# Performance work log

Measured on AMD Instinct MI355X. Metric: run time of the kernel, lower is better.

Reference implementation:

```python
import jax, jax.numpy as jnp
import numpy as np

B, S, D, DIM = 8, 4096, 1024, 512  # batch, src nodes, dst nodes, feature dim


def setup_inputs() -> dict:
    key = jax.random.key(0)
    k1, k2, k3, k4, k5 = jax.random.split(key, 5)
    scale = 1.0 / np.sqrt(DIM)
    return {
        "src_val": jax.random.normal(k1, (B, S, DIM), dtype=jnp.float32),
        "src_state": jax.random.normal(k2, (B, S), dtype=jnp.float32),
        "dst_val": jax.random.normal(k3, (B, D, DIM), dtype=jnp.float32),
        "W_route": jax.random.normal(k4, (DIM, DIM), dtype=jnp.float32) * scale,
        "W_val": jax.random.normal(k5, (DIM, DIM), dtype=jnp.float32) * scale,
    }


def reference(src_val, src_state, dst_val, W_route, W_val):
    # Pairwise route logits: bilinear bipartite attention, [B, S, D]
    inv_sqrt_d = 1.0 / jnp.sqrt(jnp.asarray(src_val.shape[-1], src_val.dtype))
    q = jnp.einsum("bsd,de->bse", src_val, W_route)
    logits = jnp.einsum("bse,bke->bsk", q, dst_val) * inv_sqrt_d
    # route compression: softmax over dst nodes (dim=-1)
    routes = jax.nn.softmax(logits, axis=-1)
    # projections
    projected_val = jnp.einsum("bsd,de->bse", src_val, W_val)  # [B, S, DIM]
    projected_state = src_state                                 # identity state proj, [B, S]
    sender_strength = jax.nn.softplus(src_state)                # [B, S]
    # weighted routing + accumulation
    weighted_routes = routes * sender_strength[..., None]       # [B, S, D]
    delta_state = jnp.einsum("bsk,bs->bk", weighted_routes, projected_state)   # [B, D]
    delta_val = jnp.einsum("bsk,bsd->bkd", weighted_routes, projected_val)     # [B, D, DIM]
    return delta_state, delta_val
```

## Files before the change

kernel.cpp:

```cpp
#include <hip/hip_runtime.h>
#include <hip/hip_fp16.h>

#define B_   8
#define S_   4096
#define DD_  1024
#define DIM_ 512
#define SCALE 0.044194173824159216f

typedef __bf16 bf16x8 __attribute__((ext_vector_type(8)));
typedef float  floatx4 __attribute__((ext_vector_type(4)));

__device__ inline unsigned short f2bf(float f) {
    union { float f; unsigned int u; } v; v.f = f;
    unsigned int r = v.u + 0x7fffu + ((v.u >> 16) & 1u);
    return (unsigned short)(r >> 16);
}
__device__ inline float bf2f(unsigned short h) {
    union { unsigned int u; float f; } v; v.u = ((unsigned int)h) << 16;
    return v.f;
}
__device__ inline uint4 cvt8(const float* __restrict__ g) {
    float4 f0 = *(const float4*)g;
    float4 f1 = *(const float4*)(g + 4);
    unsigned short tmp[8] = {f2bf(f0.x), f2bf(f0.y), f2bf(f0.z), f2bf(f0.w),
                             f2bf(f1.x), f2bf(f1.y), f2bf(f1.z), f2bf(f1.w)};
    return *(const uint4*)tmp;
}
__device__ inline void async16(unsigned short* lds, const unsigned short* g) {
    __builtin_amdgcn_global_load_lds(
        (const __attribute__((address_space(1))) void*)g,
        (__attribute__((address_space(3))) void*)lds, 16, 0, 0);
}

template <int AF32, int BF32>
__device__ inline void mainloop(unsigned short* As, unsigned short* Bs,
                                const void* Ap, size_t lda,
                                const void* Bp, size_t ldb,
                                int kIters, floatx4 (&acc)[4][4]) {
    const int t = threadIdx.x, lane = t & 63, wave = t >> 6;
    const int rA = t >> 2, cA = (t & 3) * 8;
    const int mrow = (wave >> 1) * 64, ncol = (wave & 1) * 64;
    const int fr = lane & 15, fk = (lane >> 4) * 8;

    const unsigned short* gA16 = nullptr; const float* gA32 = nullptr;
    const unsigned short* gB16 = nullptr; const float* gB32 = nullptr;
    if (AF32) gA32 = (const float*)Ap + (size_t)rA * lda + cA;
    else      gA16 = (const unsigned short*)Ap + (size_t)rA * lda + cA;
    if (BF32) gB32 = (const float*)Bp + (size_t)rA * ldb + cA;
    else      gB16 = (const unsigned short*)Bp + (size_t)rA * ldb + cA;

    unsigned short* ldsA = As + wave * 512;
    unsigned short* ldsB = Bs + wave * 512;

    for (int kt = 0; kt < kIters; ++kt) {
        if (AF32) {
            *(uint4*)&As[t * 8]        = cvt8(gA32);
            *(uint4*)&As[2048 + t * 8] = cvt8(gA32 + 64 * lda);
            gA32 += 32;
        } else {
            async16(ldsA,        gA16);
            async16(ldsA + 2048, gA16 + 64 * lda);
            gA16 += 32;
        }
        if (BF32) {
            *(uint4*)&Bs[t * 8]        = cvt8(gB32);
            *(uint4*)&Bs[2048 + t * 8] = cvt8(gB32 + 64 * ldb);
            gB32 += 32;
        } else {
            async16(ldsB,        gB16);
            async16(ldsB + 2048, gB16 + 64 * ldb);
            gB16 += 32;
        }
        __syncthreads();
        bf16x8 af[4], bfr[4];
#pragma unroll
        for (int i = 0; i < 4; ++i)
            af[i] = *(const bf16x8*)&As[(mrow + i * 16 + fr) * 32 + fk];
#pragma unroll
        for (int j = 0; j < 4; ++j)
            bfr[j] = *(const bf16x8*)&Bs[(ncol + j * 16 + fr) * 32 + fk];
#pragma unroll
        for (int i = 0; i < 4; ++i)
#pragma unroll
            for (int j = 0; j < 4; ++j)
                acc[i][j] = __builtin_amdgcn_mfma_f32_16x16x32_bf16(af[i], bfr[j],
                                                                    acc[i][j], 0, 0, 0);
        __syncthreads();
    }
}

#define EPILOGUE_COORDS                                     \
    const int lane = threadIdx.x & 63, wave = threadIdx.x >> 6; \
    const int mrow = (wave >> 1) * 64, ncol = (wave & 1) * 64;  \
    const int col = lane & 15, q = lane >> 4;

#define ACC_INIT                                            \
    floatx4 acc[4][4];                                      \
    _Pragma("unroll") for (int i = 0; i < 4; ++i)           \
        _Pragma("unroll") for (int j = 0; j < 4; ++j)       \
            acc[i][j] = (floatx4){0.f, 0.f, 0.f, 0.f};

__global__ __launch_bounds__(256) void k_prep(const float* __restrict__ dst,
                                              unsigned short* __restrict__ dstb,
                                              const float* __restrict__ Wr,
                                              const float* __restrict__ Wv,
                                              unsigned short* __restrict__ WrT,
                                              unsigned short* __restrict__ WvT) {
    __shared__ float Ts[64 * 68];
    const int t = threadIdx.x;
    if (blockIdx.x < 2048) {
        const size_t idx = ((size_t)blockIdx.x * 256 + t) * 8;
        *(uint4*)&dstb[idx] = cvt8(dst + idx);
        return;
    }
    const int n2 = blockIdx.x - 2048;
    const float* W = (n2 >> 6) ? Wv : Wr;
    unsigned short* WT = (n2 >> 6) ? WvT : WrT;
    const float scl = (n2 >> 6) ? 1.f : SCALE;
    const int d0 = (n2 & 7) * 64, e0 = ((n2 >> 3) & 7) * 64;
    {
        const int r = t >> 2, c0 = (t & 3) * 16;
        const float* g = W + (size_t)(d0 + r) * DIM_ + e0 + c0;
#pragma unroll
        for (int i = 0; i < 4; ++i)
            *(float4*)&Ts[r * 68 + c0 + i * 4] = *(const float4*)(g + i * 4);
    }
    __syncthreads();
    {
        const int rr = t >> 2, c0 = (t & 3) * 16;
        unsigned short tmp[16];
#pragma unroll
        for (int j = 0; j < 16; ++j) tmp[j] = f2bf(Ts[(c0 + j) * 68 + rr] * scl);
        unsigned short* o = WT + (size_t)(e0 + rr) * DIM_ + d0 + c0;
        *(uint4*)o = *(const uint4*)tmp;
        *(uint4*)(o + 8) = *(const uint4*)(tmp + 8);
    }
}

__global__ __launch_bounds__(256) void k_q(const float* __restrict__ src,
                                           const unsigned short* __restrict__ WrT,
                                           unsigned short* __restrict__ Qb) {
    __shared__ unsigned short As[128 * 32];
    __shared__ unsigned short Bs[128 * 32];
    const int n0 = blockIdx.x * 128, m0 = blockIdx.y * 128;
    ACC_INIT
    mainloop<1, 0>(As, Bs, src + (size_t)m0 * DIM_, DIM_,
                   WrT + (size_t)n0 * DIM_, DIM_, DIM_ / 32, acc);
    EPILOGUE_COORDS
#pragma unroll
    for (int i = 0; i < 4; ++i)
#pragma unroll
        for (int j = 0; j < 4; ++j)
#pragma unroll
            for (int r = 0; r < 4; ++r)
                Qb[(size_t)(m0 + mrow + i * 16 + q * 4 + r) * DIM_ +
                   n0 + ncol + j * 16 + col] = f2bf(acc[i][j][r]);
}

__global__ __launch_bounds__(256) void k_logitsT(const unsigned short* __restrict__ dstb,
                                                 const unsigned short* __restrict__ Qb,
                                                 unsigned short* __restrict__ LTb,
                                                 float* __restrict__ Lpart) {
    __shared__ unsigned short As[128 * 32];
    __shared__ unsigned short Bs[128 * 32];
    __shared__ float csum[8][128];
    const int n = blockIdx.x;
    const int b = n & 7;
    const int rem = n >> 3;
    const int xs = rem >> 3;
    const int yd = rem & 7;
    const int n0 = xs * 128, m0 = yd * 128;
    ACC_INIT
    mainloop<0, 0>(As, Bs,
                   dstb + (size_t)b * DD_ * DIM_ + (size_t)m0 * DIM_, DIM_,
                   Qb + (size_t)b * S_ * DIM_ + (size_t)n0 * DIM_, DIM_,
                   DIM_ / 32, acc);
    EPILOGUE_COORDS
    unsigned short* LT = LTb + (size_t)b * DD_ * S_;
    float psum[4] = {0.f, 0.f, 0.f, 0.f};
#pragma unroll
    for (int i = 0; i < 4; ++i)
#pragma unroll
        for (int j = 0; j < 4; ++j)
#pragma unroll
            for (int r = 0; r < 4; ++r) {
                float e = __expf(acc[i][j][r]);
                LT[(size_t)(m0 + mrow + i * 16 + q * 4 + r) * S_ +
                   n0 + ncol + j * 16 + col] = f2bf(e);
                psum[j] += e;
            }
    const int slice = (wave >> 1) * 4 + q;
#pragma unroll
    for (int j = 0; j < 4; ++j) csum[slice][ncol + j * 16 + col] = psum[j];
    __syncthreads();
    const int t = threadIdx.x;
    if (t < 128) {
        float v = 0.f;
#pragma unroll
        for (int k = 0; k < 8; ++k) v += csum[k][t];
        Lpart[((size_t)b * 8 + yd) * S_ + n0 + t] = v;
    }
}

__global__ __launch_bounds__(256) void k_finalize(const float* __restrict__ state,
                                                  const float* __restrict__ Lpart,
                                                  float* __restrict__ scale) {
    const int i = blockIdx.x * 256 + threadIdx.x;
    const int b = i >> 12, s = i & (S_ - 1);
    float d = 0.f;
#pragma unroll
    for (int k = 0; k < 8; ++k) d += Lpart[((size_t)b * 8 + k) * S_ + s];
    const float st = state[i];
    const float sp = (st > 15.f) ? st : log1pf(__expf(st));
    scale[i] = sp / d;
}

__global__ __launch_bounds__(256) void k_pt(const unsigned short* __restrict__ WvT,
                                            const float* __restrict__ src,
                                            const float* __restrict__ scale,
                                            unsigned short* __restrict__ PTb) {
    __shared__ unsigned short As[128 * 32];
    __shared__ unsigned short Bs[128 * 32];
    const int n0 = blockIdx.x * 128, m0 = blockIdx.y * 128, b = blockIdx.z;
    ACC_INIT
    mainloop<0, 1>(As, Bs, WvT + (size_t)m0 * DIM_, DIM_,
                   src + (size_t)b * S_ * DIM_ + (size_t)n0 * DIM_, DIM_,
                   DIM_ / 32, acc);
    EPILOGUE_COORDS
    unsigned short* PT = PTb + (size_t)b * DIM_ * S_;
    const float* sc = scale + (size_t)b * S_;
#pragma unroll
    for (int j = 0; j < 4; ++j) {
        const float scj = sc[n0 + ncol + j * 16 + col];
#pragma unroll
        for (int i = 0; i < 4; ++i)
#pragma unroll
            for (int r = 0; r < 4; ++r)
                PT[(size_t)(m0 + mrow + i * 16 + q * 4 + r) * S_ +
                   n0 + ncol + j * 16 + col] = f2bf(acc[i][j][r] * scj);
    }
}

__global__ __launch_bounds__(256) void k_dval(const unsigned short* __restrict__ LTb,
                                              const unsigned short* __restrict__ PTb,
                                              __half* __restrict__ Pp) {
    __shared__ unsigned short As[128 * 32];
    __shared__ unsigned short Bs[128 * 32];
    const int n = blockIdx.x;
    const int z = (n & 7) + 8 * (n >> 8);
    const int rem = (n >> 3) & 31;
    const int xe = rem >> 3;
    const int yd = rem & 7;
    const int b = z >> 2, ks = z & 3;
    const int n0 = xe * 128, m0 = yd * 128;
    ACC_INIT
    mainloop<0, 0>(As, Bs,
                   LTb + (size_t)b * DD_ * S_ + (size_t)m0 * S_ + ks * 1024, S_,
                   PTb + (size_t)b * DIM_ * S_ + (size_t)n0 * S_ + ks * 1024, S_,
                   1024 / 32, acc);
    EPILOGUE_COORDS
    __half* O = Pp + (size_t)ks * B_ * DD_ * DIM_ + (size_t)b * DD_ * DIM_;
#pragma unroll
    for (int i = 0; i < 4; ++i)
#pragma unroll
        for (int j = 0; j < 4; ++j)
#pragma unroll
            for (int r = 0; r < 4; ++r)
                O[(size_t)(m0 + mrow + i * 16 + q * 4 + r) * DIM_ +
                  n0 + ncol + j * 16 + col] = __float2half(acc[i][j][r]);
}

__global__ __launch_bounds__(256) void k_reduce(const __half* __restrict__ Pp,
                                                float* __restrict__ d_val) {
    const size_t idx = ((size_t)blockIdx.x * 256 + threadIdx.x) * 8;
    const size_t n = (size_t)B_ * DD_ * DIM_;
    float o[8] = {0.f, 0.f, 0.f, 0.f, 0.f, 0.f, 0.f, 0.f};
#pragma unroll
    for (int ks = 0; ks < 4; ++ks) {
        uint4 v = *(const uint4*)(Pp + (size_t)ks * n + idx);
        const __half* h = (const __half*)&v;
#pragma unroll
        for (int j = 0; j < 8; ++j) o[j] += __half2float(h[j]);
    }
    *(float4*)(d_val + idx)     = (float4){o[0], o[1], o[2], o[3]};
    *(float4*)(d_val + idx + 4) = (float4){o[4], o[5], o[6], o[7]};
}

__global__ __launch_bounds__(256) void k_dstate(const unsigned short* __restrict__ LT,
                                                const float* __restrict__ state,
                                                const float* __restrict__ scale,
                                                float* __restrict__ out) {
    const int b = blockIdx.y;
    const int dd = blockIdx.x * 4 + (threadIdx.x >> 6);
    const int lane = threadIdx.x & 63;
    const unsigned short* row = LT + (size_t)b * DD_ * S_ + (size_t)dd * S_;
    const float* st = state + (size_t)b * S_;
    const float* sc = scale + (size_t)b * S_;

    float acc = 0.f;
#pragma unroll
    for (int it = 0; it < S_ / 512; ++it) {
        const int s = it * 512 + lane * 8;
        uint4 v = *(const uint4*)(row + s);
        const unsigned short* e = (const unsigned short*)&v;
        float4 f0 = *(const float4*)(st + s);
        float4 f1 = *(const float4*)(st + s + 4);
        float4 c0 = *(const float4*)(sc + s);
        float4 c1 = *(const float4*)(sc + s + 4);
        acc += bf2f(e[0]) * f0.x * c0.x + bf2f(e[1]) * f0.y * c0.y +
               bf2f(e[2]) * f0.z * c0.z + bf2f(e[3]) * f0.w * c0.w +
               bf2f(e[4]) * f1.x * c1.x + bf2f(e[5]) * f1.y * c1.y +
               bf2f(e[6]) * f1.z * c1.z + bf2f(e[7]) * f1.w * c1.w;
    }
#pragma unroll
    for (int off = 32; off; off >>= 1) acc += __shfl_down(acc, off);
    if (lane == 0) out[(size_t)b * DD_ + dd] = acc;
}

extern "C" void kernel_launch(void* const* d_in, const int* in_sizes, int n_in,
                              void* d_out, int out_size, void* d_ws, size_t ws_size,
                              hipStream_t stream) {
    const float* src   = (const float*)d_in[0];
    const float* state = (const float*)d_in[1];
    const float* dst   = (const float*)d_in[2];
    const float* Wr    = (const float*)d_in[3];
    const float* Wv    = (const float*)d_in[4];

    unsigned short* Qb  = (unsigned short*)d_ws;
    unsigned short* PTb = Qb;
    unsigned short* LT  = Qb + (size_t)B_ * S_ * DIM_;
    unsigned short* R2  = LT + (size_t)B_ * DD_ * S_;
    unsigned short* WrT = R2;
    unsigned short* WvT = WrT + (size_t)DIM_ * DIM_;
    unsigned short* dstb = WvT + (size_t)DIM_ * DIM_;
    float* Lpart = (float*)(dstb + (size_t)B_ * DD_ * DIM_);
    float* scale = Lpart + (size_t)B_ * 8 * S_;
    __half* Pp = (__half*)R2;

    float* d_state = (float*)d_out;
    float* d_val   = (float*)d_out + B_ * DD_;

    k_prep<<<dim3(2048 + 128), 256, 0, stream>>>(dst, dstb, Wr, Wv, WrT, WvT);
    k_q<<<dim3(DIM_ / 128, (B_ * S_) / 128), 256, 0, stream>>>(src, WrT, Qb);
    k_logitsT<<<dim3(2048), 256, 0, stream>>>(dstb, Qb, LT, Lpart);
    k_finalize<<<dim3((B_ * S_) / 256), 256, 0, stream>>>(state, Lpart, scale);
    k_pt<<<dim3(S_ / 128, DIM_ / 128, B_), 256, 0, stream>>>(WvT, src, scale, PTb);
    k_dstate<<<dim3(DD_ / 4, B_), 256, 0, stream>>>(LT, state, scale, d_state);
    k_dval<<<dim3(1024), 256, 0, stream>>>(LT, PTb, Pp);
    k_reduce<<<dim3((B_ * DD_ * DIM_) / 2048), 256, 0, stream>>>(Pp, d_val);
}
```

Measured before the change: 322.3 us.

## Reassociate projections onto dst side and apply W_val after aggregation

Instead of projecting every src row through W_route, the code projects the smaller dst tensor (dst·W_routeᵀ, pre-scaled) and multiplies it against bf16 src directly. Likewise W_val is moved after the route aggregation, so the value projection runs on D rows per batch instead of S rows. The aim is to cut the FLOPs of both side GEMMs. In exchange src now needs a separate bf16 conversion pass and a scaled transpose kernel, which adds memory traffic. Workspace buffers are re-aliased, and the output buffer is reused temporarily for the softmax scale.

```diff
diff --git a/kernel.cpp b/kernel.cpp
--- a/kernel.cpp
+++ b/kernel.cpp
@@ -100,52 +100,29 @@
         _Pragma("unroll") for (int j = 0; j < 4; ++j)       \
             acc[i][j] = (floatx4){0.f, 0.f, 0.f, 0.f};
 
-__global__ __launch_bounds__(256) void k_prep(const float* __restrict__ dst,
-                                              unsigned short* __restrict__ dstb,
-                                              const float* __restrict__ Wr,
-                                              const float* __restrict__ Wv,
-                                              unsigned short* __restrict__ WrT,
-                                              unsigned short* __restrict__ WvT) {
-    __shared__ float Ts[64 * 68];
+__global__ __launch_bounds__(256) void k_prep(const float* __restrict__ src,
+                                              unsigned short* __restrict__ srcb,
+                                              const float* __restrict__ dst,
+                                              unsigned short* __restrict__ dstb) {
     const int t = threadIdx.x;
-    if (blockIdx.x < 2048) {
+    if (blockIdx.x < 8192) {
         const size_t idx = ((size_t)blockIdx.x * 256 + t) * 8;
+        *(uint4*)&srcb[idx] = cvt8(src + idx);
+    } else {
+        const size_t idx = ((size_t)(blockIdx.x - 8192) * 256 + t) * 8;
         *(uint4*)&dstb[idx] = cvt8(dst + idx);
-        return;
-    }
-    const int n2 = blockIdx.x - 2048;
-    const float* W = (n2 >> 6) ? Wv : Wr;
-    unsigned short* WT = (n2 >> 6) ? WvT : WrT;
-    const float scl = (n2 >> 6) ? 1.f : SCALE;
-    const int d0 = (n2 & 7) * 64, e0 = ((n2 >> 3) & 7) * 64;
-    {
-        const int r = t >> 2, c0 = (t & 3) * 16;
-        const float* g = W + (size_t)(d0 + r) * DIM_ + e0 + c0;
-#pragma unroll
-        for (int i = 0; i < 4; ++i)
-            *(float4*)&Ts[r * 68 + c0 + i * 4] = *(const float4*)(g + i * 4);
-    }
-    __syncthreads();
-    {
-        const int rr = t >> 2, c0 = (t & 3) * 16;
-        unsigned short tmp[16];
-#pragma unroll
-        for (int j = 0; j < 16; ++j) tmp[j] = f2bf(Ts[(c0 + j) * 68 + rr] * scl);
-        unsigned short* o = WT + (size_t)(e0 + rr) * DIM_ + d0 + c0;
-        *(uint4*)o = *(const uint4*)tmp;
-        *(uint4*)(o + 8) = *(const uint4*)(tmp + 8);
-    }
-}
-
-__global__ __launch_bounds__(256) void k_q(const float* __restrict__ src,
-                                           const unsigned short* __restrict__ WrT,
-                                           unsigned short* __restrict__ Qb) {
+    }
+}
+
+__global__ __launch_bounds__(256) void k_dstWr(const unsigned short* __restrict__ dstb,
+                                               const float* __restrict__ Wr,
+                                               unsigned short* __restrict__ DW) {
     __shared__ unsigned short As[128 * 32];
     __shared__ unsigned short Bs[128 * 32];
     const int n0 = blockIdx.x * 128, m0 = blockIdx.y * 128;
     ACC_INIT
-    mainloop<1, 0>(As, Bs, src + (size_t)m0 * DIM_, DIM_,
-                   WrT + (size_t)n0 * DIM_, DIM_, DIM_ / 32, acc);
+    mainloop<0, 1>(As, Bs, dstb + (size_t)m0 * DIM_, DIM_,
+                   Wr + (size_t)n0 * DIM_, DIM_, DIM_ / 32, acc);
     EPILOGUE_COORDS
 #pragma unroll
     for (int i = 0; i < 4; ++i)
@@ -153,12 +130,12 @@
         for (int j = 0; j < 4; ++j)
 #pragma unroll
             for (int r = 0; r < 4; ++r)
-                Qb[(size_t)(m0 + mrow + i * 16 + q * 4 + r) * DIM_ +
-                   n0 + ncol + j * 16 + col] = f2bf(acc[i][j][r]);
-}
-
-__global__ __launch_bounds__(256) void k_logitsT(const unsigned short* __restrict__ dstb,
-                                                 const unsigned short* __restrict__ Qb,
+                DW[(size_t)(m0 + mrow + i * 16 + q * 4 + r) * DIM_ +
+                   n0 + ncol + j * 16 + col] = f2bf(acc[i][j][r] * SCALE);
+}
+
+__global__ __launch_bounds__(256) void k_logitsT(const unsigned short* __restrict__ DW,
+                                                 const unsigned short* __restrict__ srcb,
                                                  unsigned short* __restrict__ LTb,
                                                  float* __restrict__ Lpart) {
     __shared__ unsigned short As[128 * 32];
@@ -172,8 +149,8 @@
     const int n0 = xs * 128, m0 = yd * 128;
     ACC_INIT
     mainloop<0, 0>(As, Bs,
-                   dstb + (size_t)b * DD_ * DIM_ + (size_t)m0 * DIM_, DIM_,
-                   Qb + (size_t)b * S_ * DIM_ + (size_t)n0 * DIM_, DIM_,
+                   DW + (size_t)b * DD_ * DIM_ + (size_t)m0 * DIM_, DIM_,
+                   srcb + (size_t)b * S_ * DIM_ + (size_t)n0 * DIM_, DIM_,
                    DIM_ / 32, acc);
     EPILOGUE_COORDS
     unsigned short* LT = LTb + (size_t)b * DD_ * S_;
@@ -215,35 +192,74 @@
     scale[i] = sp / d;
 }
 
-__global__ __launch_bounds__(256) void k_pt(const unsigned short* __restrict__ WvT,
-                                            const float* __restrict__ src,
-                                            const float* __restrict__ scale,
-                                            unsigned short* __restrict__ PTb) {
-    __shared__ unsigned short As[128 * 32];
-    __shared__ unsigned short Bs[128 * 32];
-    const int n0 = blockIdx.x * 128, m0 = blockIdx.y * 128, b = blockIdx.z;
-    ACC_INIT
-    mainloop<0, 1>(As, Bs, WvT + (size_t)m0 * DIM_, DIM_,
-                   src + (size_t)b * S_ * DIM_ + (size_t)n0 * DIM_, DIM_,
-                   DIM_ / 32, acc);
-    EPILOGUE_COORDS
-    unsigned short* PT = PTb + (size_t)b * DIM_ * S_;
+__global__ __launch_bounds__(256) void k_srcT(const unsigned short* __restrict__ srcb,
+                                              const float* __restrict__ scale,
+                                              unsigned short* __restrict__ srcST) {
+    __shared__ unsigned short Ts[64 * 65];
+    const int s0 = blockIdx.x * 64, d0 = blockIdx.y * 64, b = blockIdx.z;
+    const int t = threadIdx.x;
+    {
+        const int r = t >> 2, c0 = (t & 3) * 16;
+        const unsigned short* g =
+            srcb + (size_t)b * S_ * DIM_ + (size_t)(s0 + r) * DIM_ + d0 + c0;
+        uint4 v0 = *(const uint4*)g;
+        uint4 v1 = *(const uint4*)(g + 8);
+        const unsigned short* e0 = (const unsigned short*)&v0;
+        const unsigned short* e1 = (const unsigned short*)&v1;
+        const float sc = scale[(size_t)b * S_ + s0 + r];
+#pragma unroll
+        for (int i = 0; i < 8; ++i) {
+            Ts[r * 65 + c0 + i]     = f2bf(bf2f(e0[i]) * sc);
+            Ts[r * 65 + c0 + 8 + i] = f2bf(bf2f(e1[i]) * sc);
+        }
+    }
+    __syncthreads();
+    {
+        const int rr = t >> 2, c0 = (t & 3) * 16;
+        unsigned short tmp[16];
+#pragma unroll
+        for (int j = 0; j < 16; ++j) tmp[j] = Ts[(c0 + j) * 65 + rr];
+        unsigned short* o =
+            srcST + (size_t)b * DIM_ * S_ + (size_t)(d0 + rr) * S_ + s0 + c0;
+        *(uint4*)o = *(const uint4*)tmp;
+        *(uint4*)(o + 8) = *(const uint4*)(tmp + 8);
+    }
+}
+
+__global__ __launch_bounds__(256) void k_dstate(const unsigned short* __restrict__ LT,
+                                                const float* __restrict__ state,
+                                                const float* __restrict__ scale,
+                                                float* __restrict__ out) {
+    const int b = blockIdx.y;
+    const int dd = blockIdx.x * 4 + (threadIdx.x >> 6);
+    const int lane = threadIdx.x & 63;
+    const unsigned short* row = LT + (size_t)b * DD_ * S_ + (size_t)dd * S_;
+    const float* st = state + (size_t)b * S_;
     const float* sc = scale + (size_t)b * S_;
-#pragma unroll
-    for (int j = 0; j < 4; ++j) {
-        const float scj = sc[n0 + ncol + j * 16 + col];
-#pragma unroll
-        for (int i = 0; i < 4; ++i)
-#pragma unroll
-            for (int r = 0; r < 4; ++r)
-                PT[(size_t)(m0 + mrow + i * 16 + q * 4 + r) * S_ +
-                   n0 + ncol + j * 16 + col] = f2bf(acc[i][j][r] * scj);
-    }
-}
-
-__global__ __launch_bounds__(256) void k_dval(const unsigned short* __restrict__ LTb,
-                                              const unsigned short* __restrict__ PTb,
-                                              __half* __restrict__ Pp) {
+
+    float acc = 0.f;
+#pragma unroll
+    for (int it = 0; it < S_ / 512; ++it) {
+        const int s = it * 512 + lane * 8;
+        uint4 v = *(const uint4*)(row + s);
+        const unsigned short* e = (const unsigned short*)&v;
+        float4 f0 = *(const float4*)(st + s);
+        float4 f1 = *(const float4*)(st + s + 4);
+        float4 c0 = *(const float4*)(sc + s);
+        float4 c1 = *(const float4*)(sc + s + 4);
+        acc += bf2f(e[0]) * f0.x * c0.x + bf2f(e[1]) * f0.y * c0.y +
+               bf2f(e[2]) * f0.z * c0.z + bf2f(e[3]) * f0.w * c0.w +
+               bf2f(e[4]) * f1.x * c1.x + bf2f(e[5]) * f1.y * c1.y +
+               bf2f(e[6]) * f1.z * c1.z + bf2f(e[7]) * f1.w * c1.w;
+    }
+#pragma unroll
+    for (int off = 32; off; off >>= 1) acc += __shfl_down(acc, off);
+    if (lane == 0) out[(size_t)b * DD_ + dd] = acc;
+}
+
+__global__ __launch_bounds__(256) void k_dU(const unsigned short* __restrict__ LTb,
+                                            const unsigned short* __restrict__ srcST,
+                                            __half* __restrict__ Pp) {
     __shared__ unsigned short As[128 * 32];
     __shared__ unsigned short Bs[128 * 32];
     const int n = blockIdx.x;
@@ -256,7 +272,7 @@
     ACC_INIT
     mainloop<0, 0>(As, Bs,
                    LTb + (size_t)b * DD_ * S_ + (size_t)m0 * S_ + ks * 1024, S_,
-                   PTb + (size_t)b * DIM_ * S_ + (size_t)n0 * S_ + ks * 1024, S_,
+                   srcST + (size_t)b * DIM_ * S_ + (size_t)n0 * S_ + ks * 1024, S_,
                    1024 / 32, acc);
     EPILOGUE_COORDS
     __half* O = Pp + (size_t)ks * B_ * DD_ * DIM_ + (size_t)b * DD_ * DIM_;
@@ -270,51 +286,68 @@
                   n0 + ncol + j * 16 + col] = __float2half(acc[i][j][r]);
 }
 
-__global__ __launch_bounds__(256) void k_reduce(const __half* __restrict__ Pp,
-                                                float* __restrict__ d_val) {
-    const size_t idx = ((size_t)blockIdx.x * 256 + threadIdx.x) * 8;
-    const size_t n = (size_t)B_ * DD_ * DIM_;
-    float o[8] = {0.f, 0.f, 0.f, 0.f, 0.f, 0.f, 0.f, 0.f};
-#pragma unroll
-    for (int ks = 0; ks < 4; ++ks) {
-        uint4 v = *(const uint4*)(Pp + (size_t)ks * n + idx);
-        const __half* h = (const __half*)&v;
-#pragma unroll
-        for (int j = 0; j < 8; ++j) o[j] += __half2float(h[j]);
-    }
-    *(float4*)(d_val + idx)     = (float4){o[0], o[1], o[2], o[3]};
-    *(float4*)(d_val + idx + 4) = (float4){o[4], o[5], o[6], o[7]};
-}
-
-__global__ __launch_bounds__(256) void k_dstate(const unsigned short* __restrict__ LT,
-                                                const float* __restrict__ state,
-                                                const float* __restrict__ scale,
-                                                float* __restrict__ out) {
-    const int b = blockIdx.y;
-    const int dd = blockIdx.x * 4 + (threadIdx.x >> 6);
-    const int lane = threadIdx.x & 63;
-    const unsigned short* row = LT + (size_t)b * DD_ * S_ + (size_t)dd * S_;
-    const float* st = state + (size_t)b * S_;
-    const float* sc = scale + (size_t)b * S_;
-
-    float acc = 0.f;
-#pragma unroll
-    for (int it = 0; it < S_ / 512; ++it) {
-        const int s = it * 512 + lane * 8;
-        uint4 v = *(const uint4*)(row + s);
-        const unsigned short* e = (const unsigned short*)&v;
-        float4 f0 = *(const float4*)(st + s);
-        float4 f1 = *(const float4*)(st + s + 4);
-        float4 c0 = *(const float4*)(sc + s);
-        float4 c1 = *(const float4*)(sc + s + 4);
-        acc += bf2f(e[0]) * f0.x * c0.x + bf2f(e[1]) * f0.y * c0.y +
-               bf2f(e[2]) * f0.z * c0.z + bf2f(e[3]) * f0.w * c0.w +
-               bf2f(e[4]) * f1.x * c1.x + bf2f(e[5]) * f1.y * c1.y +
-               bf2f(e[6]) * f1.z * c1.z + bf2f(e[7]) * f1.w * c1.w;
-    }
-#pragma unroll
-    for (int off = 32; off; off >>= 1) acc += __shfl_down(acc, off);
-    if (lane == 0) out[(size_t)b * DD_ + dd] = acc;
+__global__ __launch_bounds__(256) void k_reduceU(const __half* __restrict__ Pp,
+                                                 unsigned short* __restrict__ U,
+                                                 const float* __restrict__ Wv,
+                                                 unsigned short* __restrict__ WvT) {
+    __shared__ float Ts[64 * 68];
+    const int t = threadIdx.x;
+    if (blockIdx.x < 2048) {
+        const size_t idx = ((size_t)blockIdx.x * 256 + t) * 8;
+        const size_t n = (size_t)B_ * DD_ * DIM_;
+        float o[8] = {0.f, 0.f, 0.f, 0.f, 0.f, 0.f, 0.f, 0.f};
+#pragma unroll
+        for (int ks = 0; ks < 4; ++ks) {
+            uint4 v = *(const uint4*)(Pp + (size_t)ks * n + idx);
+            const __half* h = (const __half*)&v;
+#pragma unroll
+            for (int j = 0; j < 8; ++j) o[j] += __half2float(h[j]);
+        }
+        unsigned short tmp[8];
+#pragma unroll
+        for (int j = 0; j < 8; ++j) tmp[j] = f2bf(o[j]);
+        *(uint4*)&U[idx] = *(const uint4*)tmp;
+        return;
+    }
+    const int n2 = blockIdx.x - 2048;
+    const int d0 = (n2 & 7) * 64, e0 = (n2 >> 3) * 64;
+    {
+        const int r = t >> 2, c0 = (t & 3) * 16;
+        const float* g = Wv + (size_t)(d0 + r) * DIM_ + e0 + c0;
+#pragma unroll
+        for (int i = 0; i < 4; ++i)
+            *(float4*)&Ts[r * 68 + c0 + i * 4] = *(const float4*)(g + i * 4);
+    }
+    __syncthreads();
+    {
+        const int rr = t >> 2, c0 = (t & 3) * 16;
+        unsigned short tmp[16];
+#pragma unroll
+        for (int j = 0; j < 16; ++j) tmp[j] = f2bf(Ts[(c0 + j) * 68 + rr]);
+        unsigned short* o = WvT + (size_t)(e0 + rr) * DIM_ + d0 + c0;
+        *(uint4*)o = *(const uint4*)tmp;
+        *(uint4*)(o + 8) = *(const uint4*)(tmp + 8);
+    }
+}
+
+__global__ __launch_bounds__(256) void k_dvalW(const unsigned short* __restrict__ U,
+                                               const unsigned short* __restrict__ WvT,
+                                               float* __restrict__ d_val) {
+    __shared__ unsigned short As[128 * 32];
+    __shared__ unsigned short Bs[128 * 32];
+    const int n0 = blockIdx.x * 128, m0 = blockIdx.y * 128;
+    ACC_INIT
+    mainloop<0, 0>(As, Bs, U + (size_t)m0 * DIM_, DIM_,
+                   WvT + (size_t)n0 * DIM_, DIM_, DIM_ / 32, acc);
+    EPILOGUE_COORDS
+#pragma unroll
+    for (int i = 0; i < 4; ++i)
+#pragma unroll
+        for (int j = 0; j < 4; ++j)
+#pragma unroll
+            for (int r = 0; r < 4; ++r)
+                d_val[(size_t)(m0 + mrow + i * 16 + q * 4 + r) * DIM_ +
+                      n0 + ncol + j * 16 + col] = acc[i][j][r];
 }
 
 extern "C" void kernel_launch(void* const* d_in, const int* in_sizes, int n_in,
@@ -326,26 +359,28 @@
     const float* Wr    = (const float*)d_in[3];
     const float* Wv    = (const float*)d_in[4];
 
-    unsigned short* Qb  = (unsigned short*)d_ws;
-    unsigned short* PTb = Qb;
-    unsigned short* LT  = Qb + (size_t)B_ * S_ * DIM_;
-    unsigned short* R2  = LT + (size_t)B_ * DD_ * S_;
-    unsigned short* WrT = R2;
-    unsigned short* WvT = WrT + (size_t)DIM_ * DIM_;
-    unsigned short* dstb = WvT + (size_t)DIM_ * DIM_;
-    float* Lpart = (float*)(dstb + (size_t)B_ * DD_ * DIM_);
-    float* scale = Lpart + (size_t)B_ * 8 * S_;
-    __half* Pp = (__half*)R2;
+    unsigned short* srcb = (unsigned short*)d_ws;
+    __half* Pp = (__half*)d_ws;
+    unsigned short* LT = srcb + (size_t)B_ * S_ * DIM_;
+    unsigned short* U  = LT;
+    unsigned short* WvT = U + (size_t)B_ * DD_ * DIM_;
+    unsigned short* C = LT + (size_t)B_ * DD_ * S_;
+    unsigned short* dstb = C;
+    unsigned short* DW = dstb + (size_t)B_ * DD_ * DIM_;
+    float* Lpart = (float*)(DW + (size_t)B_ * DD_ * DIM_);
+    unsigned short* srcST = C;
 
     float* d_state = (float*)d_out;
     float* d_val   = (float*)d_out + B_ * DD_;
-
-    k_prep<<<dim3(2048 + 128), 256, 0, stream>>>(dst, dstb, Wr, Wv, WrT, WvT);
-    k_q<<<dim3(DIM_ / 128, (B_ * S_) / 128), 256, 0, stream>>>(src, WrT, Qb);
-    k_logitsT<<<dim3(2048), 256, 0, stream>>>(dstb, Qb, LT, Lpart);
+    float* scale   = d_val;
+
+    k_prep<<<dim3(8192 + 2048), 256, 0, stream>>>(src, srcb, dst, dstb);
+    k_dstWr<<<dim3(DIM_ / 128, (B_ * DD_) / 128), 256, 0, stream>>>(dstb, Wr, DW);
+    k_logitsT<<<dim3(2048), 256, 0, stream>>>(DW, srcb, LT, Lpart);
     k_finalize<<<dim3((B_ * S_) / 256), 256, 0, stream>>>(state, Lpart, scale);
-    k_pt<<<dim3(S_ / 128, DIM_ / 128, B_), 256, 0, stream>>>(WvT, src, scale, PTb);
     k_dstate<<<dim3(DD_ / 4, B_), 256, 0, stream>>>(LT, state, scale, d_state);
-    k_dval<<<dim3(1024), 256, 0, stream>>>(LT, PTb, Pp);
-    k_reduce<<<dim3((B_ * DD_ * DIM_) / 2048), 256, 0, stream>>>(Pp, d_val);
-}
+    k_srcT<<<dim3(S_ / 64, DIM_ / 64, B_), 256, 0, stream>>>(srcb, scale, srcST);
+    k_dU<<<dim3(1024), 256, 0, stream>>>(LT, srcST, Pp);
+    k_reduceU<<<dim3(2048 + 64), 256, 0, stream>>>(Pp, U, Wv, WvT);
+    k_dvalW<<<dim3(DIM_ / 128, (B_ * DD_) / 128), 256, 0, stream>>>(U, WvT, d_val);
+}
```

After: 298.0 us. 1.08x faster.
